# Kernel optimization log

Hardware: AMD Instinct MI355X
Metric: run time of the kernel (lower is better)

Reference implementation:

```python
import jax, jax.numpy as jnp
from jax import lax
import numpy as np

N = 4096   # layer_size
R = 4      # displacement rank
B = 8192   # batch
STD = 0.01 # init_stddev


def setup_inputs() -> dict:
    key = jax.random.key(0)
    k1, k2, k3 = jax.random.split(key, 3)
    x = jax.random.normal(k1, (B, N), jnp.float32)
    G = jax.random.normal(k2, (R, N), jnp.float32) * STD
    H = jax.random.normal(k3, (R, N), jnp.float32) * STD
    return {"x": x, "G": G, "H": H}


def _krylov(f, V, n):
    """Krylov matrices K(Z_f, v_i) for each row v_i of V: (r, n) -> (r, n, n).
    Z_f is the shift-down matrix with corner f: (Z_f v)[0] = f*v[n-1], (Z_f v)[j] = v[j-1].
    Column k of the output is Z_f^k v_i."""
    def step(c, _):
        nxt = jnp.concatenate([f * c[:, -1:], c[:, :-1]], axis=1)
        return nxt, c
    _, cols = lax.scan(step, V, None, length=n)  # (n, r, n): k-th slice is Z_f^k V
    return jnp.transpose(cols, (1, 2, 0))        # (r, n, k)


def reference(x, G, H):
    n = G.shape[1]
    KA = _krylov(1.0, G, n)    # fn_A   = Z_mult_fn(1)
    KB = _krylov(-1.0, H, n)   # fn_B_T = Z_mult_fn(-1)
    # Stein reconstruction: W - Z_1 W Z_{-1}^T... summed series; Z_1^n = I, Z_{-1}^n = -I => factor 1/2
    W = 0.5 * jnp.einsum('rik,rjk->ij', KA, KB)  # (n, n)
    return x @ W.T
```

## Files before the change

### kernel.cpp

```cpp
#include <hip/hip_runtime.h>
#include <hip/hip_bf16.h>

#define NN 4096
#define RR 4
#define BB 8192
#define CHUNK 64
#define NCHUNK (NN / CHUNK)

typedef __bf16 bf16x8 __attribute__((ext_vector_type(8)));
typedef float f32x4 __attribute__((ext_vector_type(4)));
typedef unsigned short u16;
typedef unsigned int u32;

#define GLOBAL_AS(p) ((const __attribute__((address_space(1))) u32*)(p))
#define LDS_AS(p) ((__attribute__((address_space(3))) u32*)(p))

__device__ inline u32 pack_bf2(float lo, float hi) {
    __hip_bfloat162 h2 = __float22bfloat162_rn(make_float2(lo, hi));
    return *(u32*)&h2;
}

__global__ __launch_bounds__(256) void cast_x_kernel(const float* __restrict__ x,
                                                     u16* __restrict__ xbf) {
    size_t i = (size_t)blockIdx.x * 256 + threadIdx.x;
    const float4* x4 = (const float4*)x;
    float4 a = x4[i * 2], b = x4[i * 2 + 1];
    uint4 o = make_uint4(pack_bf2(a.x, a.y), pack_bf2(a.z, a.w),
                         pack_bf2(b.x, b.y), pack_bf2(b.z, b.w));
    *(uint4*)(xbf + i * 8) = o;
}

__global__ void ksum_kernel(const float* __restrict__ G, const float* __restrict__ H,
                            float* __restrict__ S_T) {
    int dblk = blockIdx.x & 15;
    int J = blockIdx.x >> 4;
    int d = dblk * 256 + threadIdx.x;
    int t0 = J * CHUNK;
    float acc = 0.f;
#pragma unroll 4
    for (int tt = 0; tt < CHUNK; ++tt) {
        int t = t0 + tt;
        float h0 = H[t], h1 = H[NN + t], h2 = H[2 * NN + t], h3 = H[3 * NN + t];
        int idx = (d + t) & (NN - 1);
        acc += G[idx] * h0 + G[NN + idx] * h1 + G[2 * NN + idx] * h2 + G[3 * NN + idx] * h3;
    }
    S_T[J * NN + d] = acc;
}

__global__ __launch_bounds__(128) void kprefix_kernel(const float* __restrict__ G,
                                                      const float* __restrict__ H,
                                                      const float* __restrict__ S_T,
                                                      u16* __restrict__ W) {
    __shared__ u32 tile32[64 * 33];
    u16* tile = (u16*)tile32;

    int itile = blockIdx.x >> 6;
    int J = blockIdx.x & 63;
    int i0 = itile * 64, t0 = J * CHUNK;
    int dl = threadIdx.x;
    int d = (i0 - t0 - 63 + dl) & (NN - 1);

    float pre = 0.f, tot = 0.f;
    for (int Jp = 0; Jp < NCHUNK; ++Jp) {
        float v = S_T[Jp * NN + d];
        if (Jp < J) pre += v;
        tot += v;
    }
    float acc = pre - 0.5f * tot;

#pragma unroll 4
    for (int tt = 0; tt < CHUNK; ++tt) {
        int t = t0 + tt;
        float h0 = H[t], h1 = H[NN + t], h2 = H[2 * NN + t], h3 = H[3 * NN + t];
        int idx = (d + t) & (NN - 1);
        acc += G[idx] * h0 + G[NN + idx] * h1 + G[2 * NN + idx] * h2 + G[3 * NN + idx] * h3;
        int r = dl + tt - 63;
        if ((unsigned)r < 64u) {
            __hip_bfloat16 w = __float2bfloat16(acc);
            tile[r * 66 + tt] = *(u16*)&w;
        }
    }
    __syncthreads();

    int r = threadIdx.x >> 3;
    int c8 = threadIdx.x & 7;
#pragma unroll
    for (int pass = 0; pass < 4; ++pass) {
        int rr = pass * 16 + r;
        const u32* s = &tile32[rr * 33 + c8 * 4];
        uint4 v = make_uint4(s[0], s[1], s[2], s[3]);
        *(uint4*)(W + (size_t)(i0 + rr) * NN + t0 + c8 * 8) = v;
    }
}


#define ST_A(kt, c) do { \
    const u16* s_ = srcA + (size_t)(c) * (64 * NN) + (size_t)(kt) * 64; \
    char* d_ = (char*)As + (((kt) & 1) * 32768) + ((c) * 8192) + t16; \
    __builtin_amdgcn_global_load_lds(GLOBAL_AS(s_), LDS_AS(d_), 16, 0, 0); \
    __builtin_amdgcn_global_load_lds(GLOBAL_AS(s_ + (size_t)128 * NN), LDS_AS(d_ + 16384), 16, 0, 0); \
} while (0)

#define ST_B(kt, hb) do { \
    const u16* s_ = srcB + (size_t)(hb) * (128 * NN) + (size_t)(kt) * 64; \
    char* d_ = (char*)Bs + (((kt) & 1) * 32768) + ((hb) * 16384) + t16; \
    __builtin_amdgcn_global_load_lds(GLOBAL_AS(s_), LDS_AS(d_), 16, 0, 0); \
    __builtin_amdgcn_global_load_lds(GLOBAL_AS(s_ + (size_t)64 * NN), LDS_AS(d_ + 8192), 16, 0, 0); \
} while (0)

#define AFR(cp, mi, ks) (*(const bf16x8*)(Abase + (cp) * 32768 + (mi) * 2048 + (sx ^ ((ks) << 6))))
#define BFR(cp, ni, ks) (*(const bf16x8*)(Bbase + (cp) * 32768 + (ni) * 2048 + (sx ^ ((ks) << 6))))

#define LDXA4(cp, mb) do { \
    xa[0] = AFR(cp, (mb) + 0, 0); xa[1] = AFR(cp, (mb) + 0, 1); \
    xa[2] = AFR(cp, (mb) + 1, 0); xa[3] = AFR(cp, (mb) + 1, 1); \
    xa[4] = AFR(cp, (mb) + 2, 0); xa[5] = AFR(cp, (mb) + 2, 1); \
    xa[6] = AFR(cp, (mb) + 3, 0); xa[7] = AFR(cp, (mb) + 3, 1); \
} while (0)

#define LDBQ(cp) do { \
    bq[0] = BFR(cp, 0, 0); bq[1] = BFR(cp, 0, 1); \
    bq[2] = BFR(cp, 1, 0); bq[3] = BFR(cp, 1, 1); \
    bq[4] = BFR(cp, 2, 0); bq[5] = BFR(cp, 2, 1); \
    bq[6] = BFR(cp, 3, 0); bq[7] = BFR(cp, 3, 1); \
} while (0)

#define MFMA_(a, b, c) __builtin_amdgcn_mfma_f32_16x16x32_bf16(a, b, c, 0, 0, 0)

#define MM1(mi, ni, A0, A1) do { \
    acc[mi][ni] = MFMA_(A0, bq[2 * (ni)], acc[mi][ni]); \
    acc[mi][ni] = MFMA_(A1, bq[2 * (ni) + 1], acc[mi][ni]); \
} while (0)

#define MMH(mb) do { \
    MM1((mb) + 0, 0, xa[0], xa[1]); MM1((mb) + 0, 1, xa[0], xa[1]); \
    MM1((mb) + 0, 2, xa[0], xa[1]); MM1((mb) + 0, 3, xa[0], xa[1]); \
    MM1((mb) + 1, 0, xa[2], xa[3]); MM1((mb) + 1, 1, xa[2], xa[3]); \
    MM1((mb) + 1, 2, xa[2], xa[3]); MM1((mb) + 1, 3, xa[2], xa[3]); \
    MM1((mb) + 2, 0, xa[4], xa[5]); MM1((mb) + 2, 1, xa[4], xa[5]); \
    MM1((mb) + 2, 2, xa[4], xa[5]); MM1((mb) + 2, 3, xa[4], xa[5]); \
    MM1((mb) + 3, 0, xa[6], xa[7]); MM1((mb) + 3, 1, xa[6], xa[7]); \
    MM1((mb) + 3, 2, xa[6], xa[7]); MM1((mb) + 3, 3, xa[6], xa[7]); \
} while (0)

#define VMC(n) asm volatile("s_waitcnt vmcnt(" #n ")" ::: "memory")

#define PH4(mb, READS, STAGES, WAITC) do { \
    READS; \
    STAGES; \
    WAITC; \
    __builtin_amdgcn_s_barrier(); \
    __builtin_amdgcn_s_setprio(1); \
    MMH(mb); \
    __builtin_amdgcn_s_setprio(0); \
    __builtin_amdgcn_s_barrier(); \
} while (0)

__global__ __launch_bounds__(512, 2) void gemm256_kernel(const u16* __restrict__ At,
                                                         const u16* __restrict__ Bt,
                                                         float* __restrict__ C) {
    __shared__ __align__(16) u16 As[2][2][2][64][64];
    __shared__ __align__(16) u16 Bs[2][2][2][64][64];

    int bid = blockIdx.x;
    int swz = (bid & 7) * 64 + (bid >> 3);
    int bx = swz & 15, by = swz >> 4;
    int m0 = by * 256, n0 = bx * 256;

    int t = threadIdx.x;
    int lane = t & 63, wave = t >> 6;
    int wm = wave >> 2, wn = wave & 3;
    int lrow = lane & 15, lq = lane >> 4;

    int rowt = t >> 3;
    int colel = ((t & 7) ^ (rowt & 7)) << 3;
    const u16* srcA = At + (size_t)(m0 + rowt) * NN + colel;
    const u16* srcB = Bt + (size_t)(n0 + rowt) * NN + colel;
    int t16 = t * 16;

    const char* Abase = (const char*)As + wm * 16384 + lrow * 128;
    const char* Bbase = (const char*)Bs + (wn >> 1) * 16384 + (wn & 1) * 8192 + lrow * 128;
    int sx = (lq << 4) ^ ((lrow & 7) << 4);

    f32x4 acc[8][4] = {};
    bf16x8 xa[8], bq[8];

    ST_B(0, 0); ST_B(0, 1); ST_A(0, 0); ST_A(0, 1);
    ST_B(1, 0); ST_B(1, 1); ST_A(1, 0);
    VMC(6);
    __builtin_amdgcn_s_barrier();

#pragma unroll 1
    for (int i = 0; i < 31; ++i) {
        int k0 = 2 * i;
        PH4(0, { LDBQ(0); LDXA4(0, 0); }, ST_A(k0 + 1, 1), );
        PH4(4, LDXA4(0, 4),
             { ST_B(k0 + 2, 0); ST_B(k0 + 2, 1); ST_A(k0 + 2, 0); }, VMC(6));
        PH4(0, { LDBQ(1); LDXA4(1, 0); }, ST_A(k0 + 2, 1), );
        PH4(4, LDXA4(1, 4),
             { ST_B(k0 + 3, 0); ST_B(k0 + 3, 1); ST_A(k0 + 3, 0); }, VMC(6));
    }
    PH4(0, { LDBQ(0); LDXA4(0, 0); }, ST_A(63, 1), );
    PH4(4, LDXA4(0, 4), , VMC(0));
    PH4(0, { LDBQ(1); LDXA4(1, 0); }, , );
    PH4(4, LDXA4(1, 4), , );

#pragma unroll
    for (int mi = 0; mi < 8; ++mi)
#pragma unroll
        for (int ni = 0; ni < 4; ++ni)
#pragma unroll
            for (int e = 0; e < 4; ++e) {
                int row = m0 + wm * 128 + mi * 16 + lq * 4 + e;
                int col = n0 + wn * 64 + ni * 16 + lrow;
                C[(size_t)row * NN + col] = acc[mi][ni][e];
            }
}

extern "C" void kernel_launch(void* const* d_in, const int* in_sizes, int n_in,
                              void* d_out, int out_size, void* d_ws, size_t ws_size,
                              hipStream_t stream) {
    const float* x = (const float*)d_in[0];
    const float* G = (const float*)d_in[1];
    const float* H = (const float*)d_in[2];
    float* y = (float*)d_out;

    char* ws = (char*)d_ws;
    u16* xbf = (u16*)ws;
    u16* Wbf = (u16*)(ws + (size_t)BB * NN * 2);
    float* S_T = (float*)(ws + (size_t)BB * NN * 2 + (size_t)NN * NN * 2);

    hipLaunchKernelGGL(cast_x_kernel, dim3((size_t)BB * NN / 8 / 256), dim3(256), 0, stream,
                       x, xbf);
    hipLaunchKernelGGL(ksum_kernel, dim3((NN / 256) * NCHUNK), dim3(256), 0, stream, G, H, S_T);
    hipLaunchKernelGGL(kprefix_kernel, dim3(64 * 64), dim3(128), 0, stream, G, H, S_T, Wbf);
    hipLaunchKernelGGL(gemm256_kernel, dim3((BB / 256) * (NN / 256)), dim3(512), 0, stream,
                       xbf, Wbf, y);
}
```

Before: 491.9 us.

## Replace phased barrier pipeline with one-barrier-per-tile schedule using sched_group_barrier interleave

After: 497.8 us. No clear change (+1.2%).

```diff
diff --git a/kernel.cpp b/kernel.cpp
--- a/kernel.cpp
+++ b/kernel.cpp
@@ -108,51 +108,57 @@
     __builtin_amdgcn_global_load_lds(GLOBAL_AS(s_ + (size_t)64 * NN), LDS_AS(d_ + 8192), 16, 0, 0); \
 } while (0)
 
+#define SGB __builtin_amdgcn_sched_group_barrier
+#define SG_DS(n) SGB(0x100, n, 0)
+#define SG_MM(n) SGB(0x008, n, 0)
+#define SG_VM(n) SGB(0x030, n, 0)
+
+#define ST_TILE(kt) do { \
+    ST_A(kt, 0); ST_A(kt, 1); ST_B(kt, 0); ST_B(kt, 1); SG_VM(8); \
+} while (0)
+
 #define AFR(cp, mi, ks) (*(const bf16x8*)(Abase + (cp) * 32768 + (mi) * 2048 + (sx ^ ((ks) << 6))))
 #define BFR(cp, ni, ks) (*(const bf16x8*)(Bbase + (cp) * 32768 + (ni) * 2048 + (sx ^ ((ks) << 6))))
 
-#define LDXA4(cp, mb) do { \
-    xa[0] = AFR(cp, (mb) + 0, 0); xa[1] = AFR(cp, (mb) + 0, 1); \
-    xa[2] = AFR(cp, (mb) + 1, 0); xa[3] = AFR(cp, (mb) + 1, 1); \
-    xa[4] = AFR(cp, (mb) + 2, 0); xa[5] = AFR(cp, (mb) + 2, 1); \
-    xa[6] = AFR(cp, (mb) + 3, 0); xa[7] = AFR(cp, (mb) + 3, 1); \
-} while (0)
-
-#define LDBQ(cp) do { \
+#define MFMA_(a, b, c) __builtin_amdgcn_mfma_f32_16x16x32_bf16(a, b, c, 0, 0, 0)
+
+#define MMe(mi, ni) do { \
+    acc[mi][ni] = MFMA_(xe0, bq[2 * (ni)], acc[mi][ni]); \
+    acc[mi][ni] = MFMA_(xe1, bq[2 * (ni) + 1], acc[mi][ni]); \
+} while (0)
+#define MMo(mi, ni) do { \
+    acc[mi][ni] = MFMA_(xo0, bq[2 * (ni)], acc[mi][ni]); \
+    acc[mi][ni] = MFMA_(xo1, bq[2 * (ni) + 1], acc[mi][ni]); \
+} while (0)
+
+#define VMC(n) asm volatile("s_waitcnt vmcnt(" #n ")" ::: "memory")
+
+#define TILE_BODY(cp, STAGE) do { \
+    STAGE; \
+     \
     bq[0] = BFR(cp, 0, 0); bq[1] = BFR(cp, 0, 1); \
-    bq[2] = BFR(cp, 1, 0); bq[3] = BFR(cp, 1, 1); \
+    xe0 = AFR(cp, 0, 0);   xe1 = AFR(cp, 0, 1); \
+    bq[2] = BFR(cp, 1, 0); bq[3] = BFR(cp, 1, 1); SG_DS(6); \
+     \
     bq[4] = BFR(cp, 2, 0); bq[5] = BFR(cp, 2, 1); \
-    bq[6] = BFR(cp, 3, 0); bq[7] = BFR(cp, 3, 1); \
-} while (0)
-
-#define MFMA_(a, b, c) __builtin_amdgcn_mfma_f32_16x16x32_bf16(a, b, c, 0, 0, 0)
-
-#define MM1(mi, ni, A0, A1) do { \
-    acc[mi][ni] = MFMA_(A0, bq[2 * (ni)], acc[mi][ni]); \
-    acc[mi][ni] = MFMA_(A1, bq[2 * (ni) + 1], acc[mi][ni]); \
-} while (0)
-
-#define MMH(mb) do { \
-    MM1((mb) + 0, 0, xa[0], xa[1]); MM1((mb) + 0, 1, xa[0], xa[1]); \
-    MM1((mb) + 0, 2, xa[0], xa[1]); MM1((mb) + 0, 3, xa[0], xa[1]); \
-    MM1((mb) + 1, 0, xa[2], xa[3]); MM1((mb) + 1, 1, xa[2], xa[3]); \
-    MM1((mb) + 1, 2, xa[2], xa[3]); MM1((mb) + 1, 3, xa[2], xa[3]); \
-    MM1((mb) + 2, 0, xa[4], xa[5]); MM1((mb) + 2, 1, xa[4], xa[5]); \
-    MM1((mb) + 2, 2, xa[4], xa[5]); MM1((mb) + 2, 3, xa[4], xa[5]); \
-    MM1((mb) + 3, 0, xa[6], xa[7]); MM1((mb) + 3, 1, xa[6], xa[7]); \
-    MM1((mb) + 3, 2, xa[6], xa[7]); MM1((mb) + 3, 3, xa[6], xa[7]); \
-} while (0)
-
-#define VMC(n) asm volatile("s_waitcnt vmcnt(" #n ")" ::: "memory")
-
-#define PH4(mb, READS, STAGES, WAITC) do { \
-    READS; \
-    STAGES; \
-    WAITC; \
-    __builtin_amdgcn_s_barrier(); \
-    __builtin_amdgcn_s_setprio(1); \
-    MMH(mb); \
-    __builtin_amdgcn_s_setprio(0); \
+    bq[6] = BFR(cp, 3, 0); bq[7] = BFR(cp, 3, 1); SG_DS(4); \
+      MMe(0, 0); MMe(0, 1); SG_MM(4); \
+              xo0 = AFR(cp, 1, 0); xo1 = AFR(cp, 1, 1); SG_DS(2); \
+      MMe(0, 2); MMe(0, 3); SG_MM(4); \
+              xe0 = AFR(cp, 2, 0); xe1 = AFR(cp, 2, 1); SG_DS(2); \
+              MMo(1, 0); MMo(1, 1); MMo(1, 2); MMo(1, 3); SG_MM(8); \
+              xo0 = AFR(cp, 3, 0); xo1 = AFR(cp, 3, 1); SG_DS(2); \
+              MMe(2, 0); MMe(2, 1); MMe(2, 2); MMe(2, 3); SG_MM(8); \
+              xe0 = AFR(cp, 4, 0); xe1 = AFR(cp, 4, 1); SG_DS(2); \
+              MMo(3, 0); MMo(3, 1); MMo(3, 2); MMo(3, 3); SG_MM(8); \
+              xo0 = AFR(cp, 5, 0); xo1 = AFR(cp, 5, 1); SG_DS(2); \
+              MMe(4, 0); MMe(4, 1); MMe(4, 2); MMe(4, 3); SG_MM(8); \
+              xe0 = AFR(cp, 6, 0); xe1 = AFR(cp, 6, 1); SG_DS(2); \
+              MMo(5, 0); MMo(5, 1); MMo(5, 2); MMo(5, 3); SG_MM(8); \
+              xo0 = AFR(cp, 7, 0); xo1 = AFR(cp, 7, 1); SG_DS(2); \
+              MMe(6, 0); MMe(6, 1); MMe(6, 2); MMe(6, 3); SG_MM(8); \
+              MMo(7, 0); MMo(7, 1); MMo(7, 2); MMo(7, 3); SG_MM(8); \
+    VMC(0); \
     __builtin_amdgcn_s_barrier(); \
 } while (0)
 
@@ -183,27 +189,20 @@
     int sx = (lq << 4) ^ ((lrow & 7) << 4);
 
     f32x4 acc[8][4] = {};
-    bf16x8 xa[8], bq[8];
-
-    ST_B(0, 0); ST_B(0, 1); ST_A(0, 0); ST_A(0, 1);
-    ST_B(1, 0); ST_B(1, 1); ST_A(1, 0);
-    VMC(6);
+    bf16x8 bq[8], xe0, xe1, xo0, xo1;
+
+    ST_TILE(0);
+    VMC(0);
     __builtin_amdgcn_s_barrier();
 
 #pragma unroll 1
-    for (int i = 0; i < 31; ++i) {
-        int k0 = 2 * i;
-        PH4(0, { LDBQ(0); LDXA4(0, 0); }, ST_A(k0 + 1, 1), );
-        PH4(4, LDXA4(0, 4),
-             { ST_B(k0 + 2, 0); ST_B(k0 + 2, 1); ST_A(k0 + 2, 0); }, VMC(6));
-        PH4(0, { LDBQ(1); LDXA4(1, 0); }, ST_A(k0 + 2, 1), );
-        PH4(4, LDXA4(1, 4),
-             { ST_B(k0 + 3, 0); ST_B(k0 + 3, 1); ST_A(k0 + 3, 0); }, VMC(6));
-    }
-    PH4(0, { LDBQ(0); LDXA4(0, 0); }, ST_A(63, 1), );
-    PH4(4, LDXA4(0, 4), , VMC(0));
-    PH4(0, { LDBQ(1); LDXA4(1, 0); }, , );
-    PH4(4, LDXA4(1, 4), , );
+    for (int j = 0; j < 31; ++j) {
+        int k0 = 2 * j;
+        TILE_BODY(0, ST_TILE(k0 + 1));
+        TILE_BODY(1, ST_TILE(k0 + 2));
+    }
+    TILE_BODY(0, ST_TILE(63));
+    TILE_BODY(1, );
 
 #pragma unroll
     for (int mi = 0; mi < 8; ++mi)
```
